# Kernel optimization log

Hardware: AMD Instinct MI355X
Metric: run time of the kernel (lower is better)

## Reference

```python
import jax, jax.numpy as jnp
import numpy as np

ROPE_THETA = 10000.0


def _rope(x, pos, theta):
    # x: [B, H, S, d_k], pos: [S] int. Interleaved RoPE (pairs (2i, 2i+1)).
    d_k = x.shape[-1]
    inv_freq = theta ** (-2.0 * jnp.arange(d_k // 2, dtype=jnp.float32) / d_k)  # [d_k/2]
    ang = pos.astype(jnp.float32)[:, None] * inv_freq  # [S, d_k/2]
    cos, sin = jnp.cos(ang), jnp.sin(ang)
    xe, xo = x[..., 0::2], x[..., 1::2]
    re = xe * cos - xo * sin
    ro = xe * sin + xo * cos
    return jnp.stack([re, ro], axis=-1).reshape(x.shape)


def setup_inputs() -> dict:
    key = jax.random.key(0)
    ks = jax.random.split(key, 5)
    B, S, D = 2, 2048, 1024
    return {
        "in_features": jax.random.normal(ks[0], (B, S, D), jnp.float32),
        "q_proj_weight": jax.random.normal(ks[1], (D, D), jnp.float32) * (D ** -0.5),
        "k_proj_weight": jax.random.normal(ks[2], (D, D), jnp.float32) * (D ** -0.5),
        "v_proj_weight": jax.random.normal(ks[3], (D, D), jnp.float32) * (D ** -0.5),
        "o_proj_weight": jax.random.normal(ks[4], (D, D), jnp.float32) * (D ** -0.5),
        "token_positions": jnp.arange(S, dtype=jnp.int64),
        "d_model": 1024,
        "num_heads": 16,
    }


def reference(in_features, q_proj_weight, k_proj_weight, v_proj_weight,
              o_proj_weight, token_positions, d_model, num_heads):
    B, S, _ = in_features.shape
    d_k = d_model // num_heads

    def split_heads(x):  # [B, S, D] -> [B, H, S, d_k]
        return x.reshape(B, S, num_heads, d_k).transpose(0, 2, 1, 3)

    q = split_heads(in_features @ q_proj_weight.T)
    k = split_heads(in_features @ k_proj_weight.T)
    v = split_heads(in_features @ v_proj_weight.T)

    q = _rope(q, token_positions, ROPE_THETA)
    k = _rope(k, token_positions, ROPE_THETA)

    scores = jnp.einsum("bhqd,bhkd->bhqk", q, k) / jnp.sqrt(jnp.float32(d_k))
    causal = token_positions[:, None] >= token_positions[None, :]  # [S, S]
    scores = jnp.where(causal, scores, -jnp.inf)
    probs = jax.nn.softmax(scores, axis=-1)
    ctx = jnp.einsum("bhqk,bhkd->bhqd", probs, v)  # [B, H, S, d_k]
    ctx = ctx.transpose(0, 2, 1, 3).reshape(B, S, d_model)
    return ctx @ o_proj_weight.T
```

## Files before the change

kernel.cpp:

```cpp
#include <hip/hip_runtime.h>
#include <math.h>

typedef _Float16 f16;
typedef _Float16 f16x8 __attribute__((ext_vector_type(8)));
typedef float    f32x4 __attribute__((ext_vector_type(4)));

#define SEQ  2048
#define DM   1024
#define NH   16
#define DK   64
#define MTOT 4096

#define LOG2E 1.4426950408889634f

__global__ __launch_bounds__(256)
void cvt_all(const float* __restrict__ X,  const float* __restrict__ W0,
             const float* __restrict__ W1, const float* __restrict__ W2,
             const float* __restrict__ W3, f16* __restrict__ dst)
{
    const int i = (blockIdx.x * 256 + threadIdx.x) * 4;
    const float* src;
    if (i < (4 << 20)) {
        src = X + i;
    } else {
        const int j   = i - (4 << 20);
        const int sel = j >> 20;
        const float* W = (sel == 0) ? W0 : (sel == 1) ? W1 : (sel == 2) ? W2 : W3;
        src = W + (j & ((1 << 20) - 1));
    }
    float4 v = *(const float4*)src;
    f16 o[4] = {(f16)v.x, (f16)v.y, (f16)v.z, (f16)v.w};
    *(uint2*)&dst[i] = *(const uint2*)o;
}

__global__ __launch_bounds__(512)
void gemm_qkv(const f16* __restrict__ A, const f16* __restrict__ W,
              f16* __restrict__ C)
{
    __shared__ f16 As[128][72];
    __shared__ f16 Bs[128][72];

    const int tid  = threadIdx.x;
    const int wid  = tid >> 6, lane = tid & 63;
    const int l15  = lane & 15, l4 = lane >> 4;
    const int wm   = wid >> 2, wn = wid & 3;
    const int bm   = blockIdx.x * 128;
    const int sel  = blockIdx.y >> 3;
    const int bn   = (blockIdx.y & 7) * 128;
    const f16* B   = W + ((size_t)sel << 20);
    f16* Cb        = C + ((size_t)sel << 22);

    f32x4 acc[4][2];
    #pragma unroll
    for (int mi = 0; mi < 4; ++mi)
        #pragma unroll
        for (int ni = 0; ni < 2; ++ni)
            acc[mi][ni] = (f32x4){0.f, 0.f, 0.f, 0.f};

    for (int k0 = 0; k0 < DM; k0 += 64) {
        #pragma unroll
        for (int t = 0; t < 2; ++t) {
            const int li  = tid + t * 512;
            const int row = li >> 3, c8 = (li & 7) * 8;
            *(f16x8*)&As[row][c8] = *(const f16x8*)&A[(size_t)(bm + row) * DM + k0 + c8];
            *(f16x8*)&Bs[row][c8] = *(const f16x8*)&B[(size_t)(bn + row) * DM + k0 + c8];
        }
        __syncthreads();
        #pragma unroll
        for (int kc = 0; kc < 2; ++kc) {
            f16x8 af[4], bf[2];
            #pragma unroll
            for (int mi = 0; mi < 4; ++mi)
                af[mi] = *(const f16x8*)&As[wm*64 + mi*16 + l15][kc*32 + l4*8];
            #pragma unroll
            for (int ni = 0; ni < 2; ++ni)
                bf[ni] = *(const f16x8*)&Bs[wn*32 + ni*16 + l15][kc*32 + l4*8];
            #pragma unroll
            for (int mi = 0; mi < 4; ++mi)
                #pragma unroll
                for (int ni = 0; ni < 2; ++ni)
                    acc[mi][ni] = __builtin_amdgcn_mfma_f32_16x16x32_f16(
                        af[mi], bf[ni], acc[mi][ni], 0, 0, 0);
        }
        __syncthreads();
    }

    #pragma unroll
    for (int mi = 0; mi < 4; ++mi)
        #pragma unroll
        for (int ni = 0; ni < 2; ++ni)
            #pragma unroll
            for (int r = 0; r < 4; ++r) {
                const int row = bm + wm*64 + mi*16 + l4*4 + r;
                const int col = bn + wn*32 + ni*16 + l15;
                Cb[(size_t)row * DM + col] = (f16)acc[mi][ni][r];
            }
}

__global__ __launch_bounds__(512)
void gemm_h(const f16* __restrict__ A, const f16* __restrict__ B,
            void* __restrict__ C, int f32out)
{
    __shared__ f16 As[128][72];
    __shared__ f16 Bs[128][72];

    const int tid  = threadIdx.x;
    const int wid  = tid >> 6, lane = tid & 63;
    const int l15  = lane & 15, l4 = lane >> 4;
    const int wm   = wid >> 2, wn = wid & 3;
    const int bm   = blockIdx.x * 128, bn = blockIdx.y * 128;

    f32x4 acc[4][2];
    #pragma unroll
    for (int mi = 0; mi < 4; ++mi)
        #pragma unroll
        for (int ni = 0; ni < 2; ++ni)
            acc[mi][ni] = (f32x4){0.f, 0.f, 0.f, 0.f};

    for (int k0 = 0; k0 < DM; k0 += 64) {
        #pragma unroll
        for (int t = 0; t < 2; ++t) {
            const int li  = tid + t * 512;
            const int row = li >> 3, c8 = (li & 7) * 8;
            *(f16x8*)&As[row][c8] = *(const f16x8*)&A[(size_t)(bm + row) * DM + k0 + c8];
            *(f16x8*)&Bs[row][c8] = *(const f16x8*)&B[(size_t)(bn + row) * DM + k0 + c8];
        }
        __syncthreads();
        #pragma unroll
        for (int kc = 0; kc < 2; ++kc) {
            f16x8 af[4], bf[2];
            #pragma unroll
            for (int mi = 0; mi < 4; ++mi)
                af[mi] = *(const f16x8*)&As[wm*64 + mi*16 + l15][kc*32 + l4*8];
            #pragma unroll
            for (int ni = 0; ni < 2; ++ni)
                bf[ni] = *(const f16x8*)&Bs[wn*32 + ni*16 + l15][kc*32 + l4*8];
            #pragma unroll
            for (int mi = 0; mi < 4; ++mi)
                #pragma unroll
                for (int ni = 0; ni < 2; ++ni)
                    acc[mi][ni] = __builtin_amdgcn_mfma_f32_16x16x32_f16(
                        af[mi], bf[ni], acc[mi][ni], 0, 0, 0);
        }
        __syncthreads();
    }

    #pragma unroll
    for (int mi = 0; mi < 4; ++mi)
        #pragma unroll
        for (int ni = 0; ni < 2; ++ni)
            #pragma unroll
            for (int r = 0; r < 4; ++r) {
                const int row = bm + wm*64 + mi*16 + l4*4 + r;
                const int col = bn + wn*32 + ni*16 + l15;
                const float v = acc[mi][ni][r];
                if (f32out) ((float*)C)[(size_t)row * DM + col] = v;
                else        ((f16*)  C)[(size_t)row * DM + col] = (f16)v;
            }
}

__global__ __launch_bounds__(256)
void rope_qk(f16* __restrict__ Q, f16* __restrict__ K)
{
    const int idx = blockIdx.x * 256 + threadIdx.x;
    f16* A = (idx < 524288) ? Q : K;
    const int e   = (idx & 524287) * 8;
    const int row = e >> 10;
    const int dd  = e & 63;
    const int p0  = dd >> 1;
    const float pos = (float)(row & (SEQ - 1));

    f16x8 v = *(const f16x8*)&A[e];
    f16x8 o;
    #pragma unroll
    for (int t = 0; t < 4; ++t) {
        const float freq = expf((float)(p0 + t) * -0.28782313662425575f);
        float s, c;
        sincosf(pos * freq, &s, &c);
        const float xe = (float)v[2*t], xo = (float)v[2*t + 1];
        o[2*t]     = (f16)(xe * c - xo * s);
        o[2*t + 1] = (f16)(xe * s + xo * c);
    }
    *(f16x8*)&A[e] = o;
}

__global__ __launch_bounds__(256)
void flash_mfma(const f16* __restrict__ Q, const f16* __restrict__ K,
                const f16* __restrict__ V, f16* __restrict__ O)
{
    __shared__ f16 Ks [64][72];
    __shared__ f16 Vts[64][72];
    __shared__ f16 Ps [64][72];

    const int bh  = blockIdx.y, b = bh >> 4, h = bh & 15;
    const int tid = threadIdx.x, wid = tid >> 6, lane = tid & 63;
    const int l15 = lane & 15, l4 = lane >> 4;
    const size_t base = ((size_t)b * SEQ) * DM + h * DK;

    const int srow0 = tid >> 3,        sc8 = (tid & 7) * 8;
    const int srow1 = (tid + 256) >> 3;
    const int spc0  = srow0 ^ ((tid & 7) << 3);
    const int spc1  = srow1 ^ ((tid & 7) << 3);

    f16x8 kreg[2], vreg[2];

    #pragma unroll 1
    for (int qsel = 0; qsel < 2; ++qsel) {
        const int qt = qsel ? (31 - (int)blockIdx.x) : (int)blockIdx.x;

        f16x8 qf[2];
        {
            const size_t qrow = (size_t)(qt*64 + wid*16 + l15);
            #pragma unroll
            for (int kc = 0; kc < 2; ++kc) {
                qf[kc] = *(const f16x8*)&Q[base + qrow * DM + kc*32 + l4*8];
                #pragma unroll
                for (int j = 0; j < 8; ++j)
                    qf[kc][j] = (f16)((float)qf[kc][j] * (0.125f * LOG2E));
            }
        }

        float m_r[4], l_r[4];
        f32x4 acc_o[4];
        #pragma unroll
        for (int r = 0; r < 4; ++r) { m_r[r] = -INFINITY; l_r[r] = 0.f; }
        #pragma unroll
        for (int dg = 0; dg < 4; ++dg) acc_o[dg] = (f32x4){0.f, 0.f, 0.f, 0.f};

        {
            const size_t g0 = base + (size_t)(srow0) * DM + sc8;
            const size_t g1 = base + (size_t)(srow1) * DM + sc8;
            kreg[0] = *(const f16x8*)&K[g0]; vreg[0] = *(const f16x8*)&V[g0];
            kreg[1] = *(const f16x8*)&K[g1]; vreg[1] = *(const f16x8*)&V[g1];
        }
        __syncthreads();
        *(f16x8*)&Ks[srow0][sc8] = kreg[0];
        *(f16x8*)&Ks[srow1][sc8] = kreg[1];
        #pragma unroll
        for (int j = 0; j < 8; ++j) { Vts[sc8+j][spc0] = vreg[0][j];
                                      Vts[sc8+j][spc1] = vreg[1][j]; }
        __syncthreads();

        for (int kt = 0; kt <= qt; ++kt) {
            if (kt < qt) {
                const size_t g0 = base + (size_t)((kt+1)*64 + srow0) * DM + sc8;
                const size_t g1 = base + (size_t)((kt+1)*64 + srow1) * DM + sc8;
                kreg[0] = *(const f16x8*)&K[g0]; vreg[0] = *(const f16x8*)&V[g0];
                kreg[1] = *(const f16x8*)&K[g1]; vreg[1] = *(const f16x8*)&V[g1];
            }

            f32x4 sc[4];
            #pragma unroll
            for (int cg = 0; cg < 4; ++cg) sc[cg] = (f32x4){0.f, 0.f, 0.f, 0.f};
            #pragma unroll
            for (int cg = 0; cg < 4; ++cg)
                #pragma unroll
                for (int kc = 0; kc < 2; ++kc) {
                    f16x8 bf = *(const f16x8*)&Ks[cg*16 + l15][kc*32 + l4*8];
                    sc[cg] = __builtin_amdgcn_mfma_f32_16x16x32_f16(qf[kc], bf, sc[cg], 0, 0, 0);
                }

            if (kt == qt) {
                #pragma unroll
                for (int cg = 0; cg < 4; ++cg)
                    #pragma unroll
                    for (int r = 0; r < 4; ++r)
                        if (cg*16 + l15 > wid*16 + l4*4 + r) sc[cg][r] = -INFINITY;
            }

            #pragma unroll
            for (int r = 0; r < 4; ++r) {
                float mx = fmaxf(fmaxf(sc[0][r], sc[1][r]), fmaxf(sc[2][r], sc[3][r]));
                mx = fmaxf(mx, __shfl_xor(mx, 1));
                mx = fmaxf(mx, __shfl_xor(mx, 2));
                mx = fmaxf(mx, __shfl_xor(mx, 4));
                mx = fmaxf(mx, __shfl_xor(mx, 8));
                const float mn   = fmaxf(m_r[r], mx);
                const float corr = exp2f(m_r[r] - mn);
                float ps = 0.f;
                #pragma unroll
                for (int cg = 0; cg < 4; ++cg) {
                    const float pv = exp2f(sc[cg][r] - mn);
                    sc[cg][r] = pv;
                    ps += pv;
                }
                ps += __shfl_xor(ps, 1);
                ps += __shfl_xor(ps, 2);
                ps += __shfl_xor(ps, 4);
                ps += __shfl_xor(ps, 8);
                l_r[r] = l_r[r] * corr + ps;
                m_r[r] = mn;
                #pragma unroll
                for (int dg = 0; dg < 4; ++dg) acc_o[dg][r] *= corr;
            }

            #pragma unroll
            for (int cg = 0; cg < 4; ++cg)
                #pragma unroll
                for (int r = 0; r < 4; ++r)
                    Ps[wid*16 + l4*4 + r][cg*16 + l15] = (f16)sc[cg][r];

            #pragma unroll
            for (int kc = 0; kc < 2; ++kc) {
                f16x8 pa = *(const f16x8*)&Ps[wid*16 + l15][kc*32 + l4*8];
                #pragma unroll
                for (int dg = 0; dg < 4; ++dg) {
                    const int d   = dg*16 + l15;
                    const int pcr = (kc*32 + l4*8) ^ (((d >> 3) & 7) << 3);
                    f16x8 vb = *(const f16x8*)&Vts[d][pcr];
                    acc_o[dg] = __builtin_amdgcn_mfma_f32_16x16x32_f16(pa, vb, acc_o[dg], 0, 0, 0);
                }
            }

            __syncthreads();
            if (kt < qt) {
                *(f16x8*)&Ks[srow0][sc8] = kreg[0];
                *(f16x8*)&Ks[srow1][sc8] = kreg[1];
                #pragma unroll
                for (int j = 0; j < 8; ++j) { Vts[sc8+j][spc0] = vreg[0][j];
                                              Vts[sc8+j][spc1] = vreg[1][j]; }
            }
            __syncthreads();
        }

        #pragma unroll
        for (int dg = 0; dg < 4; ++dg)
            #pragma unroll
            for (int r = 0; r < 4; ++r) {
                const size_t row = (size_t)(qt*64 + wid*16 + l4*4 + r);
                O[base + row * DM + dg*16 + l15] = (f16)(acc_o[dg][r] / l_r[r]);
            }
    }
}

extern "C" void kernel_launch(void* const* d_in, const int* in_sizes, int n_in,
                              void* d_out, int out_size, void* d_ws, size_t ws_size,
                              hipStream_t stream)
{
    const float* X  = (const float*)d_in[0];
    const float* Wq = (const float*)d_in[1];
    const float* Wk = (const float*)d_in[2];
    const float* Wv = (const float*)d_in[3];
    const float* Wo = (const float*)d_in[4];

    f16* ws = (f16*)d_ws;
    const size_t M1 = 1u << 20;
    f16* Xh  = ws;
    f16* Wqh = ws + 4*M1;
    f16* Woh = ws + 7*M1;
    f16* Qh  = ws + 8*M1;
    f16* Kh  = ws + 12*M1;
    f16* Vh  = ws + 16*M1;
    f16* Ch  = ws + 20*M1;

    cvt_all<<<8192, 256, 0, stream>>>(X, Wq, Wk, Wv, Wo, Xh);

    gemm_qkv<<<dim3(MTOT/128, 24), 512, 0, stream>>>(Xh, Wqh, Qh);

    rope_qk<<<4096, 256, 0, stream>>>(Qh, Kh);

    flash_mfma<<<dim3(16, NH*2), 256, 0, stream>>>(Qh, Kh, Vh, Ch);

    gemm_h<<<dim3(MTOT/128, DM/128), 512, 0, stream>>>(Ch, Woh, d_out, 1);
}
```

Measured before the change: 233.1 us.

## Fuse RoPE into QKV GEMM epilogue and use direct global-to-LDS loads

Drops the separate RoPE kernel. Rotation is now applied in the QKV GEMM epilogue using a precomputed cos/sin table and a lane shuffle to fetch the pair partner. Both GEMMs switch to 256-thread blocks with 64x64 per-wave tiles, load tiles with global_load_lds straight into unpadded shared memory, and gemm_h loses its runtime output-type branch. This removes a full read-modify-write pass over Q and K and the register round-trip for tile staging, at the cost of fewer waves per block and possible LDS bank conflicts from the unpadded layout.

```diff
diff --git a/kernel.cpp b/kernel.cpp
--- a/kernel.cpp
+++ b/kernel.cpp
@@ -12,6 +12,13 @@
 #define MTOT 4096
 
 #define LOG2E 1.4426950408889634f
+
+__device__ __forceinline__ void gload16(const void* g, void* l)
+{
+    __builtin_amdgcn_global_load_lds(
+        (const __attribute__((address_space(1))) void*)g,
+        (__attribute__((address_space(3))) void*)l, 16, 0, 0);
+}
 
 __global__ __launch_bounds__(256)
 void cvt_all(const float* __restrict__ X,  const float* __restrict__ W0,
@@ -33,52 +40,64 @@
     *(uint2*)&dst[i] = *(const uint2*)o;
 }
 
-__global__ __launch_bounds__(512)
+__global__ __launch_bounds__(256)
+void rope_table(float2* __restrict__ rt)
+{
+    const int i = blockIdx.x * 256 + threadIdx.x;
+    const int s = i >> 5, p = i & 31;
+    const float ang = (float)s * exp2f(-0.4152410118609203f * (float)p);
+    float sn, cs;
+    sincosf(ang, &sn, &cs);
+    rt[i] = make_float2(cs, sn);
+}
+
+__global__ __launch_bounds__(256)
 void gemm_qkv(const f16* __restrict__ A, const f16* __restrict__ W,
-              f16* __restrict__ C)
-{
-    __shared__ f16 As[128][72];
-    __shared__ f16 Bs[128][72];
-
-    const int tid  = threadIdx.x;
-    const int wid  = tid >> 6, lane = tid & 63;
-    const int l15  = lane & 15, l4 = lane >> 4;
-    const int wm   = wid >> 2, wn = wid & 3;
-    const int bm   = blockIdx.x * 128;
-    const int sel  = blockIdx.y >> 3;
-    const int bn   = (blockIdx.y & 7) * 128;
-    const f16* B   = W + ((size_t)sel << 20);
-    f16* Cb        = C + ((size_t)sel << 22);
-
-    f32x4 acc[4][2];
+              f16* __restrict__ C, const float2* __restrict__ rt)
+{
+    __shared__ f16 As[128][64];
+    __shared__ f16 Bs[128][64];
+
+    const int tid = threadIdx.x;
+    const int wid = tid >> 6, lane = tid & 63;
+    const int l15 = lane & 15, l4 = lane >> 4;
+    const int wm  = wid >> 1, wn = wid & 1;
+    const int bm  = blockIdx.x * 128;
+    const int sel = blockIdx.y >> 3;
+    const int bn  = (blockIdx.y & 7) * 128;
+    const f16* B  = W + ((size_t)sel << 20);
+    f16* Cb       = C + ((size_t)sel << 22);
+
+    const int srow = tid >> 3, scol = (tid & 7) * 8;
+
+    f32x4 acc[4][4];
     #pragma unroll
     for (int mi = 0; mi < 4; ++mi)
         #pragma unroll
-        for (int ni = 0; ni < 2; ++ni)
+        for (int ni = 0; ni < 4; ++ni)
             acc[mi][ni] = (f32x4){0.f, 0.f, 0.f, 0.f};
 
     for (int k0 = 0; k0 < DM; k0 += 64) {
         #pragma unroll
-        for (int t = 0; t < 2; ++t) {
-            const int li  = tid + t * 512;
-            const int row = li >> 3, c8 = (li & 7) * 8;
-            *(f16x8*)&As[row][c8] = *(const f16x8*)&A[(size_t)(bm + row) * DM + k0 + c8];
-            *(f16x8*)&Bs[row][c8] = *(const f16x8*)&B[(size_t)(bn + row) * DM + k0 + c8];
+        for (int i = 0; i < 4; ++i) {
+            const int row = i*32 + srow;
+            gload16(&A[(size_t)(bm + row) * DM + k0 + scol], &As[row][scol]);
+            gload16(&B[(size_t)(bn + row) * DM + k0 + scol], &Bs[row][scol]);
         }
         __syncthreads();
         #pragma unroll
         for (int kc = 0; kc < 2; ++kc) {
-            f16x8 af[4], bf[2];
+            f16x8 af[4], bf[4];
             #pragma unroll
             for (int mi = 0; mi < 4; ++mi)
                 af[mi] = *(const f16x8*)&As[wm*64 + mi*16 + l15][kc*32 + l4*8];
             #pragma unroll
-            for (int ni = 0; ni < 2; ++ni)
-                bf[ni] = *(const f16x8*)&Bs[wn*32 + ni*16 + l15][kc*32 + l4*8];
+            for (int ni = 0; ni < 4; ++ni)
+                bf[ni] = *(const f16x8*)&Bs[wn*64 + ni*16 + l15][kc*32 + l4*8];
             #pragma unroll
             for (int mi = 0; mi < 4; ++mi)
                 #pragma unroll
-                for (int ni = 0; ni < 2; ++ni)
+                for (int ni = 0; ni < 4; ++ni)
                     acc[mi][ni] = __builtin_amdgcn_mfma_f32_16x16x32_f16(
                         af[mi], bf[ni], acc[mi][ni], 0, 0, 0);
         }
@@ -88,57 +107,65 @@
     #pragma unroll
     for (int mi = 0; mi < 4; ++mi)
         #pragma unroll
-        for (int ni = 0; ni < 2; ++ni)
+        for (int ni = 0; ni < 4; ++ni)
             #pragma unroll
             for (int r = 0; r < 4; ++r) {
                 const int row = bm + wm*64 + mi*16 + l4*4 + r;
-                const int col = bn + wn*32 + ni*16 + l15;
-                Cb[(size_t)row * DM + col] = (f16)acc[mi][ni][r];
-            }
-}
-
-__global__ __launch_bounds__(512)
+                const int col = bn + wn*64 + ni*16 + l15;
+                float v = acc[mi][ni][r];
+                if (sel < 2) {
+                    const float p  = __shfl_xor(v, 1);
+                    const float2 cs = rt[((row & (SEQ-1)) << 5) | ((col & 63) >> 1)];
+                    v = (col & 1) ? fmaf(v, cs.x,  p * cs.y)
+                                  : fmaf(v, cs.x, -p * cs.y);
+                }
+                Cb[(size_t)row * DM + col] = (f16)v;
+            }
+}
+
+__global__ __launch_bounds__(256)
 void gemm_h(const f16* __restrict__ A, const f16* __restrict__ B,
-            void* __restrict__ C, int f32out)
-{
-    __shared__ f16 As[128][72];
-    __shared__ f16 Bs[128][72];
-
-    const int tid  = threadIdx.x;
-    const int wid  = tid >> 6, lane = tid & 63;
-    const int l15  = lane & 15, l4 = lane >> 4;
-    const int wm   = wid >> 2, wn = wid & 3;
-    const int bm   = blockIdx.x * 128, bn = blockIdx.y * 128;
-
-    f32x4 acc[4][2];
+            float* __restrict__ C)
+{
+    __shared__ f16 As[128][64];
+    __shared__ f16 Bs[128][64];
+
+    const int tid = threadIdx.x;
+    const int wid = tid >> 6, lane = tid & 63;
+    const int l15 = lane & 15, l4 = lane >> 4;
+    const int wm  = wid >> 1, wn = wid & 1;
+    const int bm  = blockIdx.x * 128, bn = blockIdx.y * 128;
+
+    const int srow = tid >> 3, scol = (tid & 7) * 8;
+
+    f32x4 acc[4][4];
     #pragma unroll
     for (int mi = 0; mi < 4; ++mi)
         #pragma unroll
-        for (int ni = 0; ni < 2; ++ni)
+        for (int ni = 0; ni < 4; ++ni)
             acc[mi][ni] = (f32x4){0.f, 0.f, 0.f, 0.f};
 
     for (int k0 = 0; k0 < DM; k0 += 64) {
         #pragma unroll
-        for (int t = 0; t < 2; ++t) {
-            const int li  = tid + t * 512;
-            const int row = li >> 3, c8 = (li & 7) * 8;
-            *(f16x8*)&As[row][c8] = *(const f16x8*)&A[(size_t)(bm + row) * DM + k0 + c8];
-            *(f16x8*)&Bs[row][c8] = *(const f16x8*)&B[(size_t)(bn + row) * DM + k0 + c8];
+        for (int i = 0; i < 4; ++i) {
+            const int row = i*32 + srow;
+            gload16(&A[(size_t)(bm + row) * DM + k0 + scol], &As[row][scol]);
+            gload16(&B[(size_t)(bn + row) * DM + k0 + scol], &Bs[row][scol]);
         }
         __syncthreads();
         #pragma unroll
         for (int kc = 0; kc < 2; ++kc) {
-            f16x8 af[4], bf[2];
+            f16x8 af[4], bf[4];
             #pragma unroll
             for (int mi = 0; mi < 4; ++mi)
                 af[mi] = *(const f16x8*)&As[wm*64 + mi*16 + l15][kc*32 + l4*8];
             #pragma unroll
-            for (int ni = 0; ni < 2; ++ni)
-                bf[ni] = *(const f16x8*)&Bs[wn*32 + ni*16 + l15][kc*32 + l4*8];
+            for (int ni = 0; ni < 4; ++ni)
+                bf[ni] = *(const f16x8*)&Bs[wn*64 + ni*16 + l15][kc*32 + l4*8];
             #pragma unroll
             for (int mi = 0; mi < 4; ++mi)
                 #pragma unroll
-                for (int ni = 0; ni < 2; ++ni)
+                for (int ni = 0; ni < 4; ++ni)
                     acc[mi][ni] = __builtin_amdgcn_mfma_f32_16x16x32_f16(
                         af[mi], bf[ni], acc[mi][ni], 0, 0, 0);
         }
@@ -148,40 +175,13 @@
     #pragma unroll
     for (int mi = 0; mi < 4; ++mi)
         #pragma unroll
-        for (int ni = 0; ni < 2; ++ni)
+        for (int ni = 0; ni < 4; ++ni)
             #pragma unroll
             for (int r = 0; r < 4; ++r) {
                 const int row = bm + wm*64 + mi*16 + l4*4 + r;
-                const int col = bn + wn*32 + ni*16 + l15;
-                const float v = acc[mi][ni][r];
-                if (f32out) ((float*)C)[(size_t)row * DM + col] = v;
-                else        ((f16*)  C)[(size_t)row * DM + col] = (f16)v;
-            }
-}
-
-__global__ __launch_bounds__(256)
-void rope_qk(f16* __restrict__ Q, f16* __restrict__ K)
-{
-    const int idx = blockIdx.x * 256 + threadIdx.x;
-    f16* A = (idx < 524288) ? Q : K;
-    const int e   = (idx & 524287) * 8;
-    const int row = e >> 10;
-    const int dd  = e & 63;
-    const int p0  = dd >> 1;
-    const float pos = (float)(row & (SEQ - 1));
-
-    f16x8 v = *(const f16x8*)&A[e];
-    f16x8 o;
-    #pragma unroll
-    for (int t = 0; t < 4; ++t) {
-        const float freq = expf((float)(p0 + t) * -0.28782313662425575f);
-        float s, c;
-        sincosf(pos * freq, &s, &c);
-        const float xe = (float)v[2*t], xo = (float)v[2*t + 1];
-        o[2*t]     = (f16)(xe * c - xo * s);
-        o[2*t + 1] = (f16)(xe * s + xo * c);
-    }
-    *(f16x8*)&A[e] = o;
+                const int col = bn + wn*64 + ni*16 + l15;
+                C[(size_t)row * DM + col] = acc[mi][ni][r];
+            }
 }
 
 __global__ __launch_bounds__(256)
@@ -352,14 +352,14 @@
     f16* Kh  = ws + 12*M1;
     f16* Vh  = ws + 16*M1;
     f16* Ch  = ws + 20*M1;
+    float2* rt = (float2*)(ws + 24*M1);
 
     cvt_all<<<8192, 256, 0, stream>>>(X, Wq, Wk, Wv, Wo, Xh);
-
-    gemm_qkv<<<dim3(MTOT/128, 24), 512, 0, stream>>>(Xh, Wqh, Qh);
-
-    rope_qk<<<4096, 256, 0, stream>>>(Qh, Kh);
+    rope_table<<<256, 256, 0, stream>>>(rt);
+
+    gemm_qkv<<<dim3(MTOT/128, 24), 256, 0, stream>>>(Xh, Wqh, Qh, rt);
 
     flash_mfma<<<dim3(16, NH*2), 256, 0, stream>>>(Qh, Kh, Vh, Ch);
 
-    gemm_h<<<dim3(MTOT/128, DM/128), 512, 0, stream>>>(Ch, Woh, d_out, 1);
-}
+    gemm_h<<<dim3(MTOT/128, DM/128), 256, 0, stream>>>(Ch, Woh, (float*)d_out);
+}
```

Result: slower. 254.6 us (+9.2%).
